# Kernel optimization log

Hardware: AMD Instinct MI355X
Metric: run time of the kernel (lower is better)

Reference implementation:

```python
import jax, jax.numpy as jnp
import numpy as np

N, E, C_IN, C_OUT, K = 50000, 800000, 64, 64, 3

def setup_inputs() -> dict:
    key = jax.random.key(0)
    k1, k2, k3, k4, k5, k6 = jax.random.split(key, 6)
    x = jax.random.normal(k1, (N, C_IN), dtype=jnp.float32)
    row = jax.random.randint(k2, (E,), 0, N)
    col = jax.random.randint(k3, (E,), 0, N)
    # PyG ChebConv removes self loops; avoid generating them
    col = jnp.where(col == row, (col + 1) % N, col)
    edge_index = jnp.stack([row, col])
    edge_weight = jax.random.uniform(k4, (E,), dtype=jnp.float32)
    # ChebConv learned params: one [C_in, C_out] matrix per Chebyshev order, plus bias
    W = jax.random.normal(k5, (K, C_IN, C_OUT), dtype=jnp.float32) / np.sqrt(C_IN).astype(np.float32)
    b = jax.random.normal(k6, (C_OUT,), dtype=jnp.float32) * 0.01
    return {"x": x, "edge_index": edge_index, "edge_weight": edge_weight, "W": W, "b": b}


def reference(x, edge_index, edge_weight, W, b):
    row, col = edge_index[0], edge_index[1]
    # PyG ChebConv.__norm__ with sym normalization and lambda_max = 2.0:
    # L_hat = (2/lambda_max) * (I - D^{-1/2} A D^{-1/2}) - I = -D^{-1/2} A D^{-1/2}
    deg = jax.ops.segment_sum(edge_weight, row, num_segments=N)
    dis = jnp.where(deg > 0, jax.lax.rsqrt(deg), 0.0)  # deg_inv_sqrt, inf -> 0
    w = -dis[row] * edge_weight * dis[col]             # [E] normalized Laplacian weights

    def prop(h):  # sparse matvec: L_hat @ h, [N, C]
        return jax.ops.segment_sum(w[:, None] * h[col], row, num_segments=N)

    # Chebyshev recurrence: T0 = x, T1 = L_hat x, Tk = 2 L_hat T_{k-1} - T_{k-2}
    Tx0 = x
    out = Tx0 @ W[0]
    Tx1 = prop(Tx0)
    out = out + Tx1 @ W[1]
    for k in range(2, K):
        Tx2 = 2.0 * prop(Tx1) - Tx0
        out = out + Tx2 @ W[k]
        Tx0, Tx1 = Tx1, Tx2
    return jax.nn.relu(out + b)
```

## Files before the change

### kernel.cpp

```cpp
#include <hip/hip_runtime.h>
#include <hip/hip_bf16.h>

#define C 64

typedef unsigned short u16;
typedef unsigned int u32;
typedef unsigned long long u64;

__device__ __forceinline__ u16 f2bf_rne(float v) {
    unsigned u = __float_as_uint(v);
    u += 0x7FFFu + ((u >> 16) & 1u);
    return (u16)(u >> 16);
}
__device__ __forceinline__ float bf2f(u16 u) {
    return __uint_as_float((unsigned)u << 16);
}


__global__ __launch_bounds__(256) void p1hist_kernel(const int* __restrict__ row,
                                                     u32* __restrict__ hoff,
                                                     const float* __restrict__ x,
                                                     u16* __restrict__ xh,
                                                     int E, int NB, int total4, int nthreads) {
    __shared__ u32 h[256];
    int t = threadIdx.x;
    int b = blockIdx.x;
    h[t] = 0;
    __syncthreads();
    int base = b * 1024;
#pragma unroll
    for (int u = 0; u < 4; u++) {
        int e = base + u * 256 + t;
        if (e < E) {
            int r = row[e];
            atomicAdd(&h[r >> 8], 1u);
        }
    }
    __syncthreads();
    hoff[(size_t)b * 256 + t] = h[t];

    int gtid = b * 256 + t;
    for (int i = gtid; i < total4; i += nthreads) {
        float4 v = *(const float4*)(x + (size_t)i * 4);
        ushort4 o;
        o.x = f2bf_rne(v.x); o.y = f2bf_rne(v.y);
        o.z = f2bf_rne(v.z); o.w = f2bf_rne(v.w);
        *(ushort4*)(xh + (size_t)i * 4) = o;
    }
}

__global__ __launch_bounds__(256) void scanA_kernel(u32* __restrict__ hoff,
                                                    u32* __restrict__ T, int NB) {
    __shared__ u32 s[256];
    int t = threadIdx.x;
    int d = blockIdx.x;
    u32 carry = 0;
    int nchunk = (NB + 255) / 256;
    for (int ch = 0; ch < nchunk; ch++) {
        int idx = ch * 256 + t;
        u32 v = (idx < NB) ? hoff[(size_t)idx * 256 + d] : 0;
        s[t] = v;
        __syncthreads();
        for (int off = 1; off < 256; off <<= 1) {
            u32 u = (t >= off) ? s[t - off] : 0;
            __syncthreads();
            s[t] += u;
            __syncthreads();
        }
        if (idx < NB) hoff[(size_t)idx * 256 + d] = carry + s[t] - v;
        u32 tot = s[255];
        __syncthreads();
        carry += tot;
    }
    if (t == 0) T[d] = carry;
}

__global__ __launch_bounds__(256) void scanB_kernel(const u32* __restrict__ T,
                                                    u32* __restrict__ Tpre,
                                                    int* __restrict__ rowptr, int N) {
    __shared__ u32 s[256];
    int t = threadIdx.x;
    u32 v = T[t];
    s[t] = v;
    __syncthreads();
    for (int off = 1; off < 256; off <<= 1) {
        u32 u = (t >= off) ? s[t - off] : 0;
        __syncthreads();
        s[t] += u;
        __syncthreads();
    }
    Tpre[t] = s[t] - v;
    if (t == 255) {
        Tpre[256] = s[255];
        rowptr[N] = (int)s[255];
    }
}

__global__ __launch_bounds__(256) void p1scatter_kernel(const int* __restrict__ row,
                                                        const int* __restrict__ col,
                                                        const float* __restrict__ ew,
                                                        const u32* __restrict__ hoff,
                                                        const u32* __restrict__ Tpre,
                                                        u64* __restrict__ pay,
                                                        int E) {
    __shared__ u32 cur[256];
    int t = threadIdx.x;
    int b = blockIdx.x;
    cur[t] = Tpre[t] + hoff[(size_t)b * 256 + t];
    __syncthreads();
    int base = b * 1024;
#pragma unroll
    for (int u = 0; u < 4; u++) {
        int e = base + u * 256 + t;
        if (e < E) {
            u32 r = (u32)row[e];
            u32 c = (u32)col[e];
            u32 rc = (r << 16) | c;
            u32 pos = atomicAdd(&cur[r >> 8], 1u);
            pay[pos] = ((u64)rc << 32) | (u64)__float_as_uint(ew[e]);
        }
    }
}

__global__ __launch_bounds__(256) void p2_kernel(const u64* __restrict__ pay,
                                                 const u32* __restrict__ Tpre,
                                                 int* __restrict__ rowptr,
                                                 float* __restrict__ dis,
                                                 float2* __restrict__ ewc,
                                                 int N) {
    __shared__ u32 h[256];
    __shared__ u32 s[256];
    __shared__ u32 cur[256];
    __shared__ float dsum[256];
    int t = threadIdx.x;
    int bk = blockIdx.x;
    u32 base = Tpre[bk];
    u32 cnt = Tpre[bk + 1] - base;

    h[t] = 0;
    dsum[t] = 0.0f;
    __syncthreads();
    for (u32 j = t; j < cnt; j += 256) {
        u64 v = pay[base + j];
        u32 lr = (u32)(v >> 48) & 255u;
        atomicAdd(&h[lr], 1u);
    }
    __syncthreads();
    u32 hv = h[t];
    s[t] = hv;
    __syncthreads();
    for (int off = 1; off < 256; off <<= 1) {
        u32 u = (t >= off) ? s[t - off] : 0;
        __syncthreads();
        s[t] += u;
        __syncthreads();
    }
    u32 p = s[t] - hv;
    int r = bk * 256 + t;
    if (r < N) rowptr[r] = (int)(base + p);
    cur[t] = base + p;
    __syncthreads();
    for (u32 j = t; j < cnt; j += 256) {
        u64 v = pay[base + j];
        u32 rc = (u32)(v >> 32);
        u32 lr = (rc >> 16) & 255u;
        float w = __uint_as_float((u32)v);
        u32 pos = atomicAdd(&cur[lr], 1u);
        ewc[pos] = make_float2(w, __uint_as_float(rc));
        atomicAdd(&dsum[lr], w);
    }
    __syncthreads();
    if (r < N) {
        float dv = dsum[t];
        dis[r] = (dv > 0.0f) ? rsqrtf(dv) : 0.0f;
    }
}

__global__ __launch_bounds__(256) void wnorm_kernel(float2* __restrict__ ewc,
                                                    const float* __restrict__ dis,
                                                    int E) {
    int t = threadIdx.x;
    int base = blockIdx.x * 1024;
#pragma unroll
    for (int u = 0; u < 4; u++) {
        int e = base + u * 256 + t;
        if (e < E) {
            float2 f = ewc[e];
            u32 rc = __float_as_uint(f.y);
            u32 r = rc >> 16;
            u32 c = rc & 0xffffu;
            float w = -dis[r] * f.x * dis[c];
            ewc[e] = make_float2(w, f.y);
        }
    }
}

__global__ __launch_bounds__(256) void spmm_csr_kernel(
        const int* __restrict__ rowptr,
        const float2* __restrict__ ewc,
        const unsigned* __restrict__ h32,
        float* __restrict__ out32,
        unsigned* __restrict__ outbf,
        int N) {
    int wid = (blockIdx.x * blockDim.x + threadIdx.x) >> 6;
    int lane = threadIdx.x & 63;
    if (wid >= N) return;
    int half = lane >> 5;
    int cp   = lane & 31;
    int beg = rowptr[wid];
    int end = rowptr[wid + 1];
    float ax0 = 0.f, ay0 = 0.f, ax1 = 0.f, ay1 = 0.f;
    float ax2 = 0.f, ay2 = 0.f, ax3 = 0.f, ay3 = 0.f;
    for (int base = beg; base < end; base += 64) {
        int idx = base + lane;
        float2 ed = (idx < end) ? ewc[idx] : make_float2(0.0f, __int_as_float(0));
        int cnt = end - base; if (cnt > 64) cnt = 64;
        for (int j = 0; j < cnt; j += 8) {
            int s0 = j + half;
            int s1 = j + 2 + half;
            int s2 = j + 4 + half;
            int s3 = j + 6 + half;
            float w0 = __shfl(ed.x, s0);
            int   c0 = __shfl(__float_as_int(ed.y), s0) & 0xffff;
            float w1 = __shfl(ed.x, s1);
            int   c1 = __shfl(__float_as_int(ed.y), s1) & 0xffff;
            float w2 = __shfl(ed.x, s2);
            int   c2 = __shfl(__float_as_int(ed.y), s2) & 0xffff;
            float w3 = __shfl(ed.x, s3);
            int   c3 = __shfl(__float_as_int(ed.y), s3) & 0xffff;
            unsigned hv0 = h32[(size_t)c0 * 32 + cp];
            unsigned hv1 = h32[(size_t)c1 * 32 + cp];
            unsigned hv2 = h32[(size_t)c2 * 32 + cp];
            unsigned hv3 = h32[(size_t)c3 * 32 + cp];
            ax0 = fmaf(w0, bf2f((u16)(hv0 & 0xffffu)), ax0);
            ay0 = fmaf(w0, bf2f((u16)(hv0 >> 16)),     ay0);
            ax1 = fmaf(w1, bf2f((u16)(hv1 & 0xffffu)), ax1);
            ay1 = fmaf(w1, bf2f((u16)(hv1 >> 16)),     ay1);
            ax2 = fmaf(w2, bf2f((u16)(hv2 & 0xffffu)), ax2);
            ay2 = fmaf(w2, bf2f((u16)(hv2 >> 16)),     ay2);
            ax3 = fmaf(w3, bf2f((u16)(hv3 & 0xffffu)), ax3);
            ay3 = fmaf(w3, bf2f((u16)(hv3 >> 16)),     ay3);
        }
    }
    float ax = (ax0 + ax1) + (ax2 + ax3);
    float ay = (ay0 + ay1) + (ay2 + ay3);
    float bx = __shfl(ax, cp + 32);
    float by = __shfl(ay, cp + 32);
    if (half == 0) {
        float rx = ax + bx;
        float ry = ay + by;
        *(float2*)(out32 + (size_t)wid * C + 2 * cp) = make_float2(rx, ry);
        unsigned pk = (unsigned)f2bf_rne(rx) | ((unsigned)f2bf_rne(ry) << 16);
        outbf[(size_t)wid * 32 + cp] = pk;
    }
}

__global__ __launch_bounds__(256) void final_gemm_kernel(
        const float* __restrict__ x,
        const float* __restrict__ T1,
        const float* __restrict__ P,
        const float* __restrict__ W,
        const float* __restrict__ b,
        float* __restrict__ out, int N) {
    __shared__ float As[16][64];
    __shared__ float Ws[16][64];

    int t  = threadIdx.x;
    int tx = t & 15;
    int ty = t >> 4;
    int n0 = blockIdx.x * 64;

    int sn = t >> 2;
    int skb = (t & 3) * 4;

    float acc[4][4];
#pragma unroll
    for (int i = 0; i < 4; i++)
#pragma unroll
        for (int j = 0; j < 4; j++) acc[i][j] = 0.0f;

#pragma unroll 1
    for (int s = 0; s < 12; s++) {
        float4 wv = *(const float4*)(W + s * 1024 + t * 4);
        int nn = n0 + sn;
        float4 av = make_float4(0.f, 0.f, 0.f, 0.f);
        if (nn < N) {
            if (s < 4) {
                av = *(const float4*)(x + (size_t)nn * C + s * 16 + skb);
            } else if (s < 8) {
                av = *(const float4*)(T1 + (size_t)nn * C + (s - 4) * 16 + skb);
            } else {
                float4 pv = *(const float4*)(P + (size_t)nn * C + (s - 8) * 16 + skb);
                float4 xv = *(const float4*)(x + (size_t)nn * C + (s - 8) * 16 + skb);
                av = make_float4(2.0f * pv.x - xv.x, 2.0f * pv.y - xv.y,
                                 2.0f * pv.z - xv.z, 2.0f * pv.w - xv.w);
            }
        }
        __syncthreads();
        {
            int wk = (t * 4) >> 6;
            int wc = (t * 4) & 63;
            *(float4*)&Ws[wk][wc] = wv;
        }
        As[skb + 0][sn] = av.x;
        As[skb + 1][sn] = av.y;
        As[skb + 2][sn] = av.z;
        As[skb + 3][sn] = av.w;
        __syncthreads();

#pragma unroll
        for (int kk = 0; kk < 16; kk++) {
            float4 a4 = *(const float4*)&As[kk][ty * 4];
            float4 w4 = *(const float4*)&Ws[kk][tx * 4];
            float ar[4] = {a4.x, a4.y, a4.z, a4.w};
            float wr[4] = {w4.x, w4.y, w4.z, w4.w};
#pragma unroll
            for (int i = 0; i < 4; i++)
#pragma unroll
                for (int j = 0; j < 4; j++)
                    acc[i][j] = fmaf(ar[i], wr[j], acc[i][j]);
        }
    }

    float4 bv = *(const float4*)(b + tx * 4);
    float br[4] = {bv.x, bv.y, bv.z, bv.w};
#pragma unroll
    for (int i = 0; i < 4; i++) {
        int node = n0 + ty * 4 + i;
        if (node < N) {
            float4 o;
            o.x = fmaxf(acc[i][0] + br[0], 0.0f);
            o.y = fmaxf(acc[i][1] + br[1], 0.0f);
            o.z = fmaxf(acc[i][2] + br[2], 0.0f);
            o.w = fmaxf(acc[i][3] + br[3], 0.0f);
            *(float4*)(out + (size_t)node * C + tx * 4) = o;
        }
    }
}

extern "C" void kernel_launch(void* const* d_in, const int* in_sizes, int n_in,
                              void* d_out, int out_size, void* d_ws, size_t ws_size,
                              hipStream_t stream) {
    const float* x  = (const float*)d_in[0];
    const int*   ei = (const int*)d_in[1];
    const float* ew = (const float*)d_in[2];
    const float* W  = (const float*)d_in[3];
    const float* b  = (const float*)d_in[4];
    float* out = (float*)d_out;

    const int N = in_sizes[0] / C;
    const int E = in_sizes[2];
    const int* row = ei;
    const int* col = ei + E;

    char* ws = (char*)d_ws;
    size_t off = 0;
    auto alloc = [&](size_t bytes) {
        void* p = ws + off;
        off = (off + bytes + 255) & ~(size_t)255;
        return p;
    };
    const int NB = (E + 1023) / 1024;
    const int NBUCK = (N + 255) / 256;

    float*  dis    = (float*)alloc((size_t)N * 4);
    int*    rowptr = (int*)alloc((size_t)(N + 1) * 4);
    float2* ewc    = (float2*)alloc((size_t)E * 8);
    u64*    pay    = (u64*)alloc((size_t)E * 8);
    float*  T1     = (float*)alloc((size_t)N * C * 4);
    float*  P      = (float*)alloc((size_t)N * C * 4);
    u32*    hoff   = (u32*)alloc((size_t)NB * 256 * 4);
    u32*    T      = (u32*)alloc((size_t)256 * 4);
    u32*    Tpre   = (u32*)alloc((size_t)257 * 4);
    u16*    xh     = (u16*)alloc((size_t)N * C * 2);
    u16*    T1h    = (u16*)alloc((size_t)N * C * 2);
    u16*    Ph     = (u16*)alloc((size_t)N * C * 2);

    const int B = 256;
    int total4 = N * C / 4;

    p1hist_kernel<<<NB, B, 0, stream>>>(row, hoff, x, xh, E, NB, total4, NB * B);
    scanA_kernel<<<256, B, 0, stream>>>(hoff, T, NB);
    scanB_kernel<<<1, B, 0, stream>>>(T, Tpre, rowptr, N);
    p1scatter_kernel<<<NB, B, 0, stream>>>(row, col, ew, hoff, Tpre, pay, E);
    p2_kernel<<<NBUCK, B, 0, stream>>>(pay, Tpre, rowptr, dis, ewc, N);
    wnorm_kernel<<<NB, B, 0, stream>>>(ewc, dis, E);

    int spmm_blocks = (int)(((long long)N * 64 + B - 1) / B);
    spmm_csr_kernel<<<spmm_blocks, B, 0, stream>>>(rowptr, ewc, (const unsigned*)xh,
                                                   T1, (unsigned*)T1h, N);
    spmm_csr_kernel<<<spmm_blocks, B, 0, stream>>>(rowptr, ewc, (const unsigned*)T1h,
                                                   P, (unsigned*)Ph, N);

    final_gemm_kernel<<<(N + 63) / 64, B, 0, stream>>>(x, T1, P, W, b, out, N);
}
```

Baseline: 182.6 us.

## Fuse edge-weight normalization into first SpMM and use half-wave rows

Removes the separate wnorm kernel by computing the normalized Laplacian weight inside the first SpMM pass and writing it back for the second pass. It also drops the row bits from the packed column field, and restructures the SpMM so each 32-lane half-wave handles one row. Within a row, each lane loads 8 bytes (4 bf16 channels) per edge, and edge data is staged through shared memory instead of shuffles. The aim is to save one full pass over the edge array and one launch, and to cut shuffle overhead. In exchange, the first SpMM does extra gathers of dis[c] and writes to ewc, and there is no explicit synchronisation around the shared-memory staging, which relies on wave lockstep.

New measurement: 177.1 us. 1.03x faster.

```diff
diff --git a/kernel.cpp b/kernel.cpp
--- a/kernel.cpp
+++ b/kernel.cpp
@@ -166,7 +166,7 @@
         u32 lr = (rc >> 16) & 255u;
         float w = __uint_as_float((u32)v);
         u32 pos = atomicAdd(&cur[lr], 1u);
-        ewc[pos] = make_float2(w, __uint_as_float(rc));
+        ewc[pos] = make_float2(w, __uint_as_float(rc & 0xffffu));
         atomicAdd(&dsum[lr], w);
     }
     __syncthreads();
@@ -176,82 +176,76 @@
     }
 }
 
-__global__ __launch_bounds__(256) void wnorm_kernel(float2* __restrict__ ewc,
-                                                    const float* __restrict__ dis,
-                                                    int E) {
-    int t = threadIdx.x;
-    int base = blockIdx.x * 1024;
-#pragma unroll
-    for (int u = 0; u < 4; u++) {
-        int e = base + u * 256 + t;
-        if (e < E) {
-            float2 f = ewc[e];
-            u32 rc = __float_as_uint(f.y);
-            u32 r = rc >> 16;
-            u32 c = rc & 0xffffu;
-            float w = -dis[r] * f.x * dis[c];
-            ewc[e] = make_float2(w, f.y);
-        }
-    }
-}
-
-__global__ __launch_bounds__(256) void spmm_csr_kernel(
+template <int NORM>
+__global__ __launch_bounds__(256) void spmm2_kernel(
         const int* __restrict__ rowptr,
-        const float2* __restrict__ ewc,
-        const unsigned* __restrict__ h32,
+        float2* __restrict__ ewc,
+        const float* __restrict__ dis,
+        const u64* __restrict__ h64,
         float* __restrict__ out32,
-        unsigned* __restrict__ outbf,
+        u64* __restrict__ outbf,
         int N) {
-    int wid = (blockIdx.x * blockDim.x + threadIdx.x) >> 6;
-    int lane = threadIdx.x & 63;
-    if (wid >= N) return;
-    int half = lane >> 5;
-    int cp   = lane & 31;
-    int beg = rowptr[wid];
-    int end = rowptr[wid + 1];
-    float ax0 = 0.f, ay0 = 0.f, ax1 = 0.f, ay1 = 0.f;
-    float ax2 = 0.f, ay2 = 0.f, ax3 = 0.f, ay3 = 0.f;
-    for (int base = beg; base < end; base += 64) {
-        int idx = base + lane;
-        float2 ed = (idx < end) ? ewc[idx] : make_float2(0.0f, __int_as_float(0));
-        int cnt = end - base; if (cnt > 64) cnt = 64;
-        for (int j = 0; j < cnt; j += 8) {
-            int s0 = j + half;
-            int s1 = j + 2 + half;
-            int s2 = j + 4 + half;
-            int s3 = j + 6 + half;
-            float w0 = __shfl(ed.x, s0);
-            int   c0 = __shfl(__float_as_int(ed.y), s0) & 0xffff;
-            float w1 = __shfl(ed.x, s1);
-            int   c1 = __shfl(__float_as_int(ed.y), s1) & 0xffff;
-            float w2 = __shfl(ed.x, s2);
-            int   c2 = __shfl(__float_as_int(ed.y), s2) & 0xffff;
-            float w3 = __shfl(ed.x, s3);
-            int   c3 = __shfl(__float_as_int(ed.y), s3) & 0xffff;
-            unsigned hv0 = h32[(size_t)c0 * 32 + cp];
-            unsigned hv1 = h32[(size_t)c1 * 32 + cp];
-            unsigned hv2 = h32[(size_t)c2 * 32 + cp];
-            unsigned hv3 = h32[(size_t)c3 * 32 + cp];
-            ax0 = fmaf(w0, bf2f((u16)(hv0 & 0xffffu)), ax0);
-            ay0 = fmaf(w0, bf2f((u16)(hv0 >> 16)),     ay0);
-            ax1 = fmaf(w1, bf2f((u16)(hv1 & 0xffffu)), ax1);
-            ay1 = fmaf(w1, bf2f((u16)(hv1 >> 16)),     ay1);
-            ax2 = fmaf(w2, bf2f((u16)(hv2 & 0xffffu)), ax2);
-            ay2 = fmaf(w2, bf2f((u16)(hv2 >> 16)),     ay2);
-            ax3 = fmaf(w3, bf2f((u16)(hv3 & 0xffffu)), ax3);
-            ay3 = fmaf(w3, bf2f((u16)(hv3 >> 16)),     ay3);
-        }
-    }
-    float ax = (ax0 + ax1) + (ax2 + ax3);
-    float ay = (ay0 + ay1) + (ay2 + ay3);
-    float bx = __shfl(ax, cp + 32);
-    float by = __shfl(ay, cp + 32);
-    if (half == 0) {
-        float rx = ax + bx;
-        float ry = ay + by;
-        *(float2*)(out32 + (size_t)wid * C + 2 * cp) = make_float2(rx, ry);
-        unsigned pk = (unsigned)f2bf_rne(rx) | ((unsigned)f2bf_rne(ry) << 16);
-        outbf[(size_t)wid * 32 + cp] = pk;
+    __shared__ float2 eds[8][32];
+
+    int tid  = threadIdx.x;
+    int hw   = tid >> 5;
+    int l32  = tid & 31;
+    int e2   = l32 >> 4;
+    int cq   = l32 & 15;
+
+    int row = blockIdx.x * 8 + hw;
+    if (row >= N) return;
+
+    int beg = rowptr[row];
+    int end = rowptr[row + 1];
+    float disr = NORM ? dis[row] : 0.0f;
+
+    float a0 = 0.f, a1 = 0.f, a2 = 0.f, a3 = 0.f;
+
+    for (int base = beg; base < end; base += 32) {
+        int idx = base + l32;
+        bool valid = idx < end;
+        float2 ed = valid ? ewc[idx] : make_float2(0.0f, __uint_as_float(0));
+        if (NORM) {
+            u32 c = __float_as_uint(ed.y);
+            float w = -disr * ed.x * dis[c];
+            ed = make_float2(w, __uint_as_float(c));
+            if (valid) ewc[idx] = ed;
+        }
+        eds[hw][l32] = ed;
+        int cnt = end - base; if (cnt > 32) cnt = 32;
+        for (int j = 0; j < cnt; j += 4) {
+            float2 f0 = eds[hw][j + e2];
+            float2 f1 = eds[hw][j + 2 + e2];
+            u32 c0 = __float_as_uint(f0.y);
+            u32 c1 = __float_as_uint(f1.y);
+            u64 hv0 = h64[(size_t)c0 * 16 + cq];
+            u64 hv1 = h64[(size_t)c1 * 16 + cq];
+            float w0 = f0.x, w1 = f1.x;
+            u32 lo0 = (u32)hv0, hi0 = (u32)(hv0 >> 32);
+            u32 lo1 = (u32)hv1, hi1 = (u32)(hv1 >> 32);
+            a0 = fmaf(w0, bf2f((u16)(lo0 & 0xffffu)), a0);
+            a1 = fmaf(w0, bf2f((u16)(lo0 >> 16)),     a1);
+            a2 = fmaf(w0, bf2f((u16)(hi0 & 0xffffu)), a2);
+            a3 = fmaf(w0, bf2f((u16)(hi0 >> 16)),     a3);
+            a0 = fmaf(w1, bf2f((u16)(lo1 & 0xffffu)), a0);
+            a1 = fmaf(w1, bf2f((u16)(lo1 >> 16)),     a1);
+            a2 = fmaf(w1, bf2f((u16)(hi1 & 0xffffu)), a2);
+            a3 = fmaf(w1, bf2f((u16)(hi1 >> 16)),     a3);
+        }
+    }
+
+    a0 += __shfl_xor(a0, 16);
+    a1 += __shfl_xor(a1, 16);
+    a2 += __shfl_xor(a2, 16);
+    a3 += __shfl_xor(a3, 16);
+
+    if (e2 == 0) {
+        float4 o = make_float4(a0, a1, a2, a3);
+        *(float4*)(out32 + (size_t)row * C + 4 * cq) = o;
+        u32 p0 = (u32)f2bf_rne(a0) | ((u32)f2bf_rne(a1) << 16);
+        u32 p1 = (u32)f2bf_rne(a2) | ((u32)f2bf_rne(a3) << 16);
+        outbf[(size_t)row * 16 + cq] = (u64)p0 | ((u64)p1 << 32);
     }
 }
 
@@ -384,13 +378,12 @@
     scanB_kernel<<<1, B, 0, stream>>>(T, Tpre, rowptr, N);
     p1scatter_kernel<<<NB, B, 0, stream>>>(row, col, ew, hoff, Tpre, pay, E);
     p2_kernel<<<NBUCK, B, 0, stream>>>(pay, Tpre, rowptr, dis, ewc, N);
-    wnorm_kernel<<<NB, B, 0, stream>>>(ewc, dis, E);
-
-    int spmm_blocks = (int)(((long long)N * 64 + B - 1) / B);
-    spmm_csr_kernel<<<spmm_blocks, B, 0, stream>>>(rowptr, ewc, (const unsigned*)xh,
-                                                   T1, (unsigned*)T1h, N);
-    spmm_csr_kernel<<<spmm_blocks, B, 0, stream>>>(rowptr, ewc, (const unsigned*)T1h,
-                                                   P, (unsigned*)Ph, N);
+
+    int spmm_blocks = (N + 7) / 8;
+    spmm2_kernel<1><<<spmm_blocks, B, 0, stream>>>(rowptr, ewc, dis, (const u64*)xh,
+                                                   T1, (u64*)T1h, N);
+    spmm2_kernel<0><<<spmm_blocks, B, 0, stream>>>(rowptr, ewc, dis, (const u64*)T1h,
+                                                   P, (u64*)Ph, N);
 
     final_gemm_kernel<<<(N + 63) / 64, B, 0, stream>>>(x, T1, P, W, b, out, N);
 }
```
